# Kernel tuning notes

Measured on AMD Instinct MI355X. Metric: run time of the kernel, lower is better.

Reference implementation:

```python
import jax, jax.numpy as jnp
import numpy as np

N_NODES = 100000
N_EDGES = 1600000
IN_CH, HID_CH, OUT_CH = 128, 64, 40


def setup_inputs() -> dict:
    key = jax.random.key(0)
    k_x, k_e, k_w1, k_w2 = jax.random.split(key, 4)
    x = jax.random.normal(k_x, (N_NODES, IN_CH), dtype=jnp.float32)
    edge_index = jax.random.randint(k_e, (2, N_EDGES), 0, N_NODES, dtype=jnp.int64)
    # Glorot-ish scaled weights, zero bias (matches GCNConv init convention)
    W1 = jax.random.normal(k_w1, (IN_CH, HID_CH), dtype=jnp.float32) / np.sqrt(IN_CH)
    b1 = jnp.zeros((HID_CH,), dtype=jnp.float32)
    W2 = jax.random.normal(k_w2, (HID_CH, OUT_CH), dtype=jnp.float32) / np.sqrt(HID_CH)
    b2 = jnp.zeros((OUT_CH,), dtype=jnp.float32)
    return {"x": x, "edge_index": edge_index, "W1": W1, "b1": b1, "W2": W2, "b2": b2}


def _gcn_conv(x, edge_index, W, b, n):
    """GCNConv with normalize=True: linear transform, add self-loops,
    symmetric D^-1/2 A D^-1/2 aggregation (source_to_target flow), bias."""
    h = x @ W  # [n, out]
    loops = jnp.arange(n, dtype=edge_index.dtype)
    row = jnp.concatenate([edge_index[0], loops])  # sources
    col = jnp.concatenate([edge_index[1], loops])  # targets
    deg = jax.ops.segment_sum(jnp.ones_like(col, dtype=h.dtype), col, num_segments=n)
    dinv = jnp.where(deg > 0, jax.lax.rsqrt(deg), jnp.zeros_like(deg))
    w = dinv[row] * dinv[col]  # [E+n] per-edge norm
    out = jax.ops.segment_sum(h[row] * w[:, None], col, num_segments=n)  # scatter-add to targets
    return out + b


def reference(x, edge_index, W1, b1, W2, b2):
    # eval mode: F.dropout(p=0.8, training=False) is identity
    n = x.shape[0]
    h = jax.nn.relu(_gcn_conv(x, edge_index, W1, b1, n))
    return _gcn_conv(h, edge_index, W2, b2, n)  # [N, OUT_CH] logits
```

## Files before the change

### kernel.cpp

```cpp
#include <hip/hip_runtime.h>

#define N_NODES 100000
#define NPAD    100032
#define N_EDGES 1600000
#define IN_CH   128
#define HID_CH  64
#define OUT_CH  40
#define NBKT    196
#define EPB     4096
#define CAP     9216
#define CAPC    10752

using bf16x8 = __attribute__((ext_vector_type(8))) short;
using f32x4  = __attribute__((ext_vector_type(4))) float;

__device__ __forceinline__ float bf2f(unsigned short u) {
    union { unsigned int i; float f; } c; c.i = ((unsigned int)u) << 16; return c.f;
}
__device__ __forceinline__ unsigned short f2bf(float f) {
    union { float f; unsigned int i; } c; c.f = f;
    unsigned int r = c.i + 0x7FFFu + ((c.i >> 16) & 1u);
    return (unsigned short)(r >> 16);
}
__device__ __forceinline__ float4 bf2f4(ushort4 u) {
    return make_float4(bf2f(u.x), bf2f(u.y), bf2f(u.z), bf2f(u.w));
}

__global__ void k_bin(const int* __restrict__ ei, int* __restrict__ gcur,
                      int* __restrict__ ebuf) {
    __shared__ int hist[NBKT];
    __shared__ int lcur[NBKT];
    int tid = threadIdx.x;
    int base = blockIdx.x * EPB;
    int nloc = N_EDGES - base;
    if (nloc > EPB) nloc = EPB;
    int n4 = nloc >> 2;
    const int4* S4 = (const int4*)(ei + base);
    const int4* D4 = (const int4*)(ei + N_EDGES + base);

    if (tid < NBKT) { hist[tid] = 0; }
    __syncthreads();
    for (int i = tid; i < n4; i += 256) {
        int4 d = D4[i];
        atomicAdd(&hist[d.x >> 9], 1);
        atomicAdd(&hist[d.y >> 9], 1);
        atomicAdd(&hist[d.z >> 9], 1);
        atomicAdd(&hist[d.w >> 9], 1);
    }
    __syncthreads();
    if (tid < NBKT) {
        int h = hist[tid];
        lcur[tid] = h ? (tid * CAP + atomicAdd(&gcur[tid], h)) : 0;
    }
    __syncthreads();
    for (int i = tid; i < n4; i += 256) {
        int4 s = S4[i];
        int4 d = D4[i];
        int p;
        p = atomicAdd(&lcur[d.x >> 9], 1); ebuf[p] = s.x | ((d.x & 511) << 17);
        p = atomicAdd(&lcur[d.y >> 9], 1); ebuf[p] = s.y | ((d.y & 511) << 17);
        p = atomicAdd(&lcur[d.z >> 9], 1); ebuf[p] = s.z | ((d.z & 511) << 17);
        p = atomicAdd(&lcur[d.w >> 9], 1); ebuf[p] = s.w | ((d.w & 511) << 17);
    }
}

__global__ void k_node(const int* __restrict__ gcur, const int* __restrict__ ebuf,
                       int* __restrict__ row_start, int* __restrict__ row_end,
                       int* __restrict__ csr_src, float* __restrict__ dinv) {
    __shared__ int cnt[512];
    __shared__ int s[512];
    int tid = threadIdx.x;
    int b = blockIdx.x;
    int node0 = b << 9;
    int lo = b * CAP;
    int lo2 = b * CAPC;
    int hi = lo + gcur[b];
    int n = hi - lo, n4 = n >> 2;
    const int4* E4 = (const int4*)(ebuf + lo);

    cnt[tid] = 0;
    __syncthreads();
    for (int i = tid; i < n4; i += 512) {
        int4 w = E4[i];
        atomicAdd(&cnt[(unsigned)w.x >> 17], 1);
        atomicAdd(&cnt[(unsigned)w.y >> 17], 1);
        atomicAdd(&cnt[(unsigned)w.z >> 17], 1);
        atomicAdd(&cnt[(unsigned)w.w >> 17], 1);
    }
    for (int e = lo + (n4 << 2) + tid; e < hi; e += 512)
        atomicAdd(&cnt[(unsigned)ebuf[e] >> 17], 1);
    __syncthreads();
    int c = cnt[tid];
    int cp = (c + 7) & ~7;
    s[tid] = cp;
    __syncthreads();
#pragma unroll
    for (int off = 1; off < 512; off <<= 1) {
        int tv = (tid >= off) ? s[tid - off] : 0;
        __syncthreads();
        s[tid] += tv;
        __syncthreads();
    }
    int nodestart = lo2 + s[tid] - cp;
    int node = node0 + tid;
    if (node < N_NODES) {
        row_start[node] = nodestart;
        row_end[node]   = nodestart + c;
        dinv[node] = rsqrtf(1.0f + (float)c);
    }
    __syncthreads();
    cnt[tid] = nodestart;
    __syncthreads();
    for (int i = tid; i < n4; i += 512) {
        int4 w = E4[i];
        int p;
        p = atomicAdd(&cnt[(unsigned)w.x >> 17], 1); csr_src[p] = w.x & 0x1FFFF;
        p = atomicAdd(&cnt[(unsigned)w.y >> 17], 1); csr_src[p] = w.y & 0x1FFFF;
        p = atomicAdd(&cnt[(unsigned)w.z >> 17], 1); csr_src[p] = w.z & 0x1FFFF;
        p = atomicAdd(&cnt[(unsigned)w.w >> 17], 1); csr_src[p] = w.w & 0x1FFFF;
    }
    for (int e = lo + (n4 << 2) + tid; e < hi; e += 512) {
        int w = ebuf[e];
        int p = atomicAdd(&cnt[(unsigned)w >> 17], 1);
        csr_src[p] = w & 0x1FFFF;
    }
    for (int p = nodestart + c; p < nodestart + cp; ++p)
        csr_src[p] = N_NODES;
}

__global__ __launch_bounds__(256, 4)
void k_gemm1(const float* __restrict__ x, const float* __restrict__ W1,
             const float* __restrict__ dinv, unsigned short* __restrict__ h1s) {
    __shared__ unsigned short Bl[64 * 136];
    __shared__ float dl[64];
    int tid = threadIdx.x;
    long long node0 = (long long)blockIdx.x * 64;

    for (int i = tid; i < 128 * 64; i += 256) {
        int k = i >> 6, nn = i & 63;
        Bl[nn * 136 + k] = f2bf(W1[i]);
    }
    if (tid < 64) {
        long long gr = node0 + tid;
        dl[tid] = dinv[gr < N_NODES ? gr : N_NODES - 1];
    }
    __syncthreads();

    int lane = tid & 63, wave = tid >> 6;
    int quad = lane >> 4, l16 = lane & 15;
    int arow = wave * 16 + l16;
    long long ga = node0 + arow;
    if (ga >= N_NODES) ga = N_NODES - 1;
    const float* xr = x + ga * IN_CH;
    f32x4 ac0 = {0,0,0,0}, ac1 = {0,0,0,0}, ac2 = {0,0,0,0}, ac3 = {0,0,0,0};

#pragma unroll
    for (int ks = 0; ks < 4; ++ks) {
        int ko = ks * 32 + quad * 8;
        float4 xa = *(const float4*)&xr[ko];
        float4 xb = *(const float4*)&xr[ko + 4];
        bf16x8 a;
        a[0] = (short)f2bf(xa.x); a[1] = (short)f2bf(xa.y);
        a[2] = (short)f2bf(xa.z); a[3] = (short)f2bf(xa.w);
        a[4] = (short)f2bf(xb.x); a[5] = (short)f2bf(xb.y);
        a[6] = (short)f2bf(xb.z); a[7] = (short)f2bf(xb.w);
        bf16x8 b0 = *(const bf16x8*)&Bl[( 0 + l16) * 136 + ko];
        bf16x8 b1 = *(const bf16x8*)&Bl[(16 + l16) * 136 + ko];
        bf16x8 b2 = *(const bf16x8*)&Bl[(32 + l16) * 136 + ko];
        bf16x8 b3 = *(const bf16x8*)&Bl[(48 + l16) * 136 + ko];
        ac0 = __builtin_amdgcn_mfma_f32_16x16x32_bf16(a, b0, ac0, 0, 0, 0);
        ac1 = __builtin_amdgcn_mfma_f32_16x16x32_bf16(a, b1, ac1, 0, 0, 0);
        ac2 = __builtin_amdgcn_mfma_f32_16x16x32_bf16(a, b2, ac2, 0, 0, 0);
        ac3 = __builtin_amdgcn_mfma_f32_16x16x32_bf16(a, b3, ac3, 0, 0, 0);
    }

#pragma unroll
    for (int r = 0; r < 4; ++r) {
        int rl = wave * 16 + quad * 4 + r;
        long long grow = node0 + rl;
        if (grow < N_NODES) {
            float dd = dl[rl];
            h1s[grow * 64 +  0 + l16] = f2bf(ac0[r] * dd);
            h1s[grow * 64 + 16 + l16] = f2bf(ac1[r] * dd);
            h1s[grow * 64 + 32 + l16] = f2bf(ac2[r] * dd);
            h1s[grow * 64 + 48 + l16] = f2bf(ac3[r] * dd);
        } else {
            h1s[grow * 64 +  0 + l16] = 0;
            h1s[grow * 64 + 16 + l16] = 0;
            h1s[grow * 64 + 32 + l16] = 0;
            h1s[grow * 64 + 48 + l16] = 0;
        }
    }
}

__global__ __launch_bounds__(256, 4)
void k_agg1g2(const int* __restrict__ row_start, const int* __restrict__ row_end,
              const int* __restrict__ csr_src,
              const unsigned short* __restrict__ h1s, const float* __restrict__ dinv,
              const float* __restrict__ b1, const float* __restrict__ W2,
              unsigned short* __restrict__ h2s) {
    __shared__ unsigned short Al[32 * 72];
    __shared__ unsigned short Bl[48 * 72];
    __shared__ float dl[32];
    int tid = threadIdx.x;
    long long node0 = (long long)blockIdx.x * 32;

    for (int i = tid; i < 48 * 64; i += 256) {
        int nn = i >> 6, k = i & 63;
        Bl[nn * 72 + k] = f2bf(nn < OUT_CH ? W2[k * OUT_CH + nn] : 0.0f);
    }
    if (tid < 32) {
        long long gr = node0 + tid;
        dl[tid] = dinv[gr < N_NODES ? gr : N_NODES - 1];
    }
    __syncthreads();

    int g  = tid >> 4;
    int hh = (tid >> 3) & 1;
    int c8 = tid & 7;
    int nl = g * 2 + hh;
    long long node = node0 + nl;

    int e0 = 0, d = 0;
    if (node < N_NODES) { e0 = row_start[node]; d = row_end[node] - e0; }
    int len8 = (d + 7) & ~7;
    int lenO = __shfl_xor(len8, 8, 16);
    int nIt  = (len8 > lenO ? len8 : lenO) >> 3;

    float4 aA = {0.f,0.f,0.f,0.f}, aB = aA, aC = aA, aD = aA;

    int it = 0;
    while (it < nIt) {
        bool real = (it << 3) < len8;
        int base = real ? (e0 + (it << 3)) : e0;
        int idxr = csr_src[base + c8];
        int s0 = __shfl(idxr, 0, 8), s1 = __shfl(idxr, 1, 8);
        int s2 = __shfl(idxr, 2, 8), s3 = __shfl(idxr, 3, 8);
        int s4 = __shfl(idxr, 4, 8), s5 = __shfl(idxr, 5, 8);
        int s6 = __shfl(idxr, 6, 8), s7 = __shfl(idxr, 7, 8);
        if (!real) { s0=s1=s2=s3=s4=s5=s6=s7 = N_NODES; }
        const unsigned short* Hc = h1s + (long long)c8 * 8;
        bf16x8 r0 = *(const bf16x8*)&Hc[(long long)s0 * 64];
        bf16x8 r1 = *(const bf16x8*)&Hc[(long long)s1 * 64];
        bf16x8 r2 = *(const bf16x8*)&Hc[(long long)s2 * 64];
        bf16x8 r3 = *(const bf16x8*)&Hc[(long long)s3 * 64];
        bf16x8 r4 = *(const bf16x8*)&Hc[(long long)s4 * 64];
        bf16x8 r5 = *(const bf16x8*)&Hc[(long long)s5 * 64];
        bf16x8 r6 = *(const bf16x8*)&Hc[(long long)s6 * 64];
        bf16x8 r7 = *(const bf16x8*)&Hc[(long long)s7 * 64];
#define ACC8(R, LO, HI) { \
        LO.x += bf2f((unsigned short)R[0]); LO.y += bf2f((unsigned short)R[1]); \
        LO.z += bf2f((unsigned short)R[2]); LO.w += bf2f((unsigned short)R[3]); \
        HI.x += bf2f((unsigned short)R[4]); HI.y += bf2f((unsigned short)R[5]); \
        HI.z += bf2f((unsigned short)R[6]); HI.w += bf2f((unsigned short)R[7]); }
        ACC8(r0, aA, aB) ACC8(r1, aC, aD)
        ACC8(r2, aA, aB) ACC8(r3, aC, aD)
        ACC8(r4, aA, aB) ACC8(r5, aC, aD)
        ACC8(r6, aA, aB) ACC8(r7, aC, aD)
#undef ACC8
        ++it;
    }
    aA.x += aC.x; aA.y += aC.y; aA.z += aC.z; aA.w += aC.w;
    aB.x += aD.x; aB.y += aD.y; aB.z += aD.z; aB.w += aD.w;

    bf16x8 res = {0,0,0,0,0,0,0,0};
    if (node < N_NODES) {
        bf16x8 sv = *(const bf16x8*)&h1s[(long long)node * 64 + c8 * 8];
        aA.x += bf2f((unsigned short)sv[0]); aA.y += bf2f((unsigned short)sv[1]);
        aA.z += bf2f((unsigned short)sv[2]); aA.w += bf2f((unsigned short)sv[3]);
        aB.x += bf2f((unsigned short)sv[4]); aB.y += bf2f((unsigned short)sv[5]);
        aB.z += bf2f((unsigned short)sv[6]); aB.w += bf2f((unsigned short)sv[7]);
        float dd = dl[nl];
        float4 blo = ((const float4*)b1)[c8 * 2];
        float4 bhi = ((const float4*)b1)[c8 * 2 + 1];
        res[0] = (short)f2bf(fmaxf(aA.x * dd + blo.x, 0.f));
        res[1] = (short)f2bf(fmaxf(aA.y * dd + blo.y, 0.f));
        res[2] = (short)f2bf(fmaxf(aA.z * dd + blo.z, 0.f));
        res[3] = (short)f2bf(fmaxf(aA.w * dd + blo.w, 0.f));
        res[4] = (short)f2bf(fmaxf(aB.x * dd + bhi.x, 0.f));
        res[5] = (short)f2bf(fmaxf(aB.y * dd + bhi.y, 0.f));
        res[6] = (short)f2bf(fmaxf(aB.z * dd + bhi.z, 0.f));
        res[7] = (short)f2bf(fmaxf(aB.w * dd + bhi.w, 0.f));
    }
    *(bf16x8*)&Al[nl * 72 + c8 * 8] = res;
    __syncthreads();

    int lane = tid & 63, wave = tid >> 6;
    if (wave < 2) {
        int quad = lane >> 4, l16 = lane & 15;
        int arow = wave * 16 + l16;
        f32x4 ac0 = {0,0,0,0}, ac1 = {0,0,0,0}, ac2 = {0,0,0,0};

#pragma unroll
        for (int ks = 0; ks < 2; ++ks) {
            int ko = ks * 32 + quad * 8;
            bf16x8 a  = *(const bf16x8*)&Al[arow * 72 + ko];
            bf16x8 b0 = *(const bf16x8*)&Bl[( 0 + l16) * 72 + ko];
            bf16x8 b1v = *(const bf16x8*)&Bl[(16 + l16) * 72 + ko];
            bf16x8 b2 = *(const bf16x8*)&Bl[(32 + l16) * 72 + ko];
            ac0 = __builtin_amdgcn_mfma_f32_16x16x32_bf16(a, b0, ac0, 0, 0, 0);
            ac1 = __builtin_amdgcn_mfma_f32_16x16x32_bf16(a, b1v, ac1, 0, 0, 0);
            ac2 = __builtin_amdgcn_mfma_f32_16x16x32_bf16(a, b2, ac2, 0, 0, 0);
        }

#pragma unroll
        for (int r = 0; r < 4; ++r) {
            int rl = wave * 16 + quad * 4 + r;
            long long grow = node0 + rl;
            if (grow < N_NODES) {
                float dd = dl[rl];
                h2s[grow * 40 +  0 + l16] = f2bf(ac0[r] * dd);
                h2s[grow * 40 + 16 + l16] = f2bf(ac1[r] * dd);
                if (l16 < 8) h2s[grow * 40 + 32 + l16] = f2bf(ac2[r] * dd);
            } else if (grow < NPAD) {
                h2s[grow * 40 +  0 + l16] = 0;
                h2s[grow * 40 + 16 + l16] = 0;
                if (l16 < 8) h2s[grow * 40 + 32 + l16] = 0;
            }
        }
    }
}

__global__ void k_agg2(const int* __restrict__ row_start, const int* __restrict__ row_end,
                       const int* __restrict__ csr_src,
                       const unsigned short* __restrict__ h2s, const float* __restrict__ dinv,
                       const float* __restrict__ b2, float* __restrict__ out) {
    int idx = blockIdx.x * blockDim.x + threadIdx.x;
    int node = idx >> 4;
    int cg = idx & 15;
    if (node >= N_NODES || cg >= 10) return;
    int e = row_start[node];
    int f = row_end[node];
    int f8 = e + ((f - e + 7) & ~7);
    const ushort4* H = (const ushort4*)h2s;
    float4 acc = bf2f4(H[(long long)node * 10 + cg]);
    float4 acc2 = {0.f, 0.f, 0.f, 0.f};
    while (e < f8) {
        int s0 = csr_src[e];
        int s1 = csr_src[e + 1];
        int s2 = csr_src[e + 2];
        int s3 = csr_src[e + 3];
        int s4 = csr_src[e + 4];
        int s5 = csr_src[e + 5];
        int s6 = csr_src[e + 6];
        int s7 = csr_src[e + 7];
        float4 v0 = bf2f4(H[(long long)s0 * 10 + cg]);
        float4 v1 = bf2f4(H[(long long)s1 * 10 + cg]);
        float4 v2 = bf2f4(H[(long long)s2 * 10 + cg]);
        float4 v3 = bf2f4(H[(long long)s3 * 10 + cg]);
        float4 u0 = bf2f4(H[(long long)s4 * 10 + cg]);
        float4 u1 = bf2f4(H[(long long)s5 * 10 + cg]);
        float4 u2 = bf2f4(H[(long long)s6 * 10 + cg]);
        float4 u3 = bf2f4(H[(long long)s7 * 10 + cg]);
        acc.x  += (v0.x + v1.x) + (v2.x + v3.x);
        acc.y  += (v0.y + v1.y) + (v2.y + v3.y);
        acc.z  += (v0.z + v1.z) + (v2.z + v3.z);
        acc.w  += (v0.w + v1.w) + (v2.w + v3.w);
        acc2.x += (u0.x + u1.x) + (u2.x + u3.x);
        acc2.y += (u0.y + u1.y) + (u2.y + u3.y);
        acc2.z += (u0.z + u1.z) + (u2.z + u3.z);
        acc2.w += (u0.w + u1.w) + (u2.w + u3.w);
        e += 8;
    }
    acc.x += acc2.x; acc.y += acc2.y; acc.z += acc2.z; acc.w += acc2.w;
    float dd = dinv[node];
    float4 b = ((const float4*)b2)[cg];
    acc.x = acc.x * dd + b.x;
    acc.y = acc.y * dd + b.y;
    acc.z = acc.z * dd + b.z;
    acc.w = acc.w * dd + b.w;
    ((float4*)out)[(long long)node * 10 + cg] = acc;
}

extern "C" void kernel_launch(void* const* d_in, const int* in_sizes, int n_in,
                              void* d_out, int out_size, void* d_ws, size_t ws_size,
                              hipStream_t stream) {
    const float* x  = (const float*)d_in[0];
    const int*   ei = (const int*)d_in[1];
    const float* W1 = (const float*)d_in[2];
    const float* b1 = (const float*)d_in[3];
    const float* W2 = (const float*)d_in[4];
    const float* b2 = (const float*)d_in[5];
    float* out = (float*)d_out;

    unsigned short* hbuf  = (unsigned short*)d_ws;
    unsigned short* h2buf = hbuf + 64LL * NPAD;
    int* ebuf      = (int*)(h2buf + 40LL * NPAD);
    int* csr_src   = ebuf + NBKT * CAP;
    int* row_start = csr_src + NBKT * CAPC + 64;
    int* row_end   = row_start + N_NODES;
    int* gcur      = row_end + N_NODES;
    float* dinv    = (float*)(gcur + 256);

    const int B = 256;
    const int g16 = (N_NODES * 16 + B - 1) / B;
    const int gRows = NPAD / 64;
    const int gAgg  = NPAD / 32;

    hipMemsetAsync((void*)gcur, 0, NBKT * sizeof(int), stream);
    k_bin<<<(N_EDGES + EPB - 1) / EPB, B, 0, stream>>>(ei, gcur, ebuf);
    k_node<<<NBKT, 512, 0, stream>>>(gcur, ebuf, row_start, row_end, csr_src, dinv);

    k_gemm1<<<gRows, B, 0, stream>>>(x, W1, dinv, hbuf);
    k_agg1g2<<<gAgg, B, 0, stream>>>(row_start, row_end, csr_src, hbuf, dinv,
                                     b1, W2, h2buf);
    k_agg2<<<g16, B, 0, stream>>>(row_start, row_end, csr_src, h2buf, dinv, b2, out);
}
```

Measured before the change: 215.8 us.

## Restructure layer-2 aggregation with 16-byte gathers and shuffled edge indices

Rewrites k_agg2 so each node uses 8 lanes, 5 of them active, and each lane loads 8 bf16 values (16 bytes) instead of 4. The lanes load 8 neighbour indices cooperatively in one coalesced read and broadcast them with width-8 shuffles, so each lane no longer fetches every index itself. Two nodes share a 16-lane group and loop to the longer of their two edge counts, so the shorter node issues padded dummy gathers. Those dummy loads, and the ones from the 3 idle lanes, point at the zeroed padding row N_NODES, so they add nothing to the sums. Block count drops to NPAD/32 blocks of 32 nodes, with launch bounds added.

Result: no change. 215.1 us (-0.3%).

```diff
diff --git a/kernel.cpp b/kernel.cpp
--- a/kernel.cpp
+++ b/kernel.cpp
@@ -321,55 +321,84 @@
     }
 }
 
-__global__ void k_agg2(const int* __restrict__ row_start, const int* __restrict__ row_end,
-                       const int* __restrict__ csr_src,
-                       const unsigned short* __restrict__ h2s, const float* __restrict__ dinv,
-                       const float* __restrict__ b2, float* __restrict__ out) {
-    int idx = blockIdx.x * blockDim.x + threadIdx.x;
-    int node = idx >> 4;
-    int cg = idx & 15;
-    if (node >= N_NODES || cg >= 10) return;
-    int e = row_start[node];
-    int f = row_end[node];
-    int f8 = e + ((f - e + 7) & ~7);
-    const ushort4* H = (const ushort4*)h2s;
-    float4 acc = bf2f4(H[(long long)node * 10 + cg]);
-    float4 acc2 = {0.f, 0.f, 0.f, 0.f};
-    while (e < f8) {
-        int s0 = csr_src[e];
-        int s1 = csr_src[e + 1];
-        int s2 = csr_src[e + 2];
-        int s3 = csr_src[e + 3];
-        int s4 = csr_src[e + 4];
-        int s5 = csr_src[e + 5];
-        int s6 = csr_src[e + 6];
-        int s7 = csr_src[e + 7];
-        float4 v0 = bf2f4(H[(long long)s0 * 10 + cg]);
-        float4 v1 = bf2f4(H[(long long)s1 * 10 + cg]);
-        float4 v2 = bf2f4(H[(long long)s2 * 10 + cg]);
-        float4 v3 = bf2f4(H[(long long)s3 * 10 + cg]);
-        float4 u0 = bf2f4(H[(long long)s4 * 10 + cg]);
-        float4 u1 = bf2f4(H[(long long)s5 * 10 + cg]);
-        float4 u2 = bf2f4(H[(long long)s6 * 10 + cg]);
-        float4 u3 = bf2f4(H[(long long)s7 * 10 + cg]);
-        acc.x  += (v0.x + v1.x) + (v2.x + v3.x);
-        acc.y  += (v0.y + v1.y) + (v2.y + v3.y);
-        acc.z  += (v0.z + v1.z) + (v2.z + v3.z);
-        acc.w  += (v0.w + v1.w) + (v2.w + v3.w);
-        acc2.x += (u0.x + u1.x) + (u2.x + u3.x);
-        acc2.y += (u0.y + u1.y) + (u2.y + u3.y);
-        acc2.z += (u0.z + u1.z) + (u2.z + u3.z);
-        acc2.w += (u0.w + u1.w) + (u2.w + u3.w);
-        e += 8;
-    }
-    acc.x += acc2.x; acc.y += acc2.y; acc.z += acc2.z; acc.w += acc2.w;
-    float dd = dinv[node];
-    float4 b = ((const float4*)b2)[cg];
-    acc.x = acc.x * dd + b.x;
-    acc.y = acc.y * dd + b.y;
-    acc.z = acc.z * dd + b.z;
-    acc.w = acc.w * dd + b.w;
-    ((float4*)out)[(long long)node * 10 + cg] = acc;
+__global__ __launch_bounds__(256, 4)
+void k_agg2(const int* __restrict__ row_start, const int* __restrict__ row_end,
+            const int* __restrict__ csr_src,
+            const unsigned short* __restrict__ h2s, const float* __restrict__ dinv,
+            const float* __restrict__ b2, float* __restrict__ out) {
+    int tid = threadIdx.x;
+    long long node0 = (long long)blockIdx.x * 32;
+
+    int g  = tid >> 4;
+    int hh = (tid >> 3) & 1;
+    int c8 = tid & 7;
+    int nl = g * 2 + hh;
+    long long node = node0 + nl;
+    bool act = c8 < 5;
+
+    int e0 = 0, d = 0;
+    if (node < N_NODES) { e0 = row_start[node]; d = row_end[node] - e0; }
+    int len8 = (d + 7) & ~7;
+    int lenO = __shfl_xor(len8, 8, 16);
+    int nIt  = (len8 > lenO ? len8 : lenO) >> 3;
+
+    const unsigned short* Hb = h2s + (act ? (long long)c8 * 8
+                                          : (long long)N_NODES * 40);
+    long long rmul = act ? 40LL : 0LL;
+
+    float4 aA = {0.f,0.f,0.f,0.f}, aB = aA, aC = aA, aD = aA;
+
+    int it = 0;
+    while (it < nIt) {
+        bool real = (it << 3) < len8;
+        int base = real ? (e0 + (it << 3)) : e0;
+        int idxr = csr_src[base + c8];
+        int s0 = __shfl(idxr, 0, 8), s1 = __shfl(idxr, 1, 8);
+        int s2 = __shfl(idxr, 2, 8), s3 = __shfl(idxr, 3, 8);
+        int s4 = __shfl(idxr, 4, 8), s5 = __shfl(idxr, 5, 8);
+        int s6 = __shfl(idxr, 6, 8), s7 = __shfl(idxr, 7, 8);
+        if (!real) { s0=s1=s2=s3=s4=s5=s6=s7 = N_NODES; }
+        bf16x8 r0 = *(const bf16x8*)&Hb[(long long)s0 * rmul];
+        bf16x8 r1 = *(const bf16x8*)&Hb[(long long)s1 * rmul];
+        bf16x8 r2 = *(const bf16x8*)&Hb[(long long)s2 * rmul];
+        bf16x8 r3 = *(const bf16x8*)&Hb[(long long)s3 * rmul];
+        bf16x8 r4 = *(const bf16x8*)&Hb[(long long)s4 * rmul];
+        bf16x8 r5 = *(const bf16x8*)&Hb[(long long)s5 * rmul];
+        bf16x8 r6 = *(const bf16x8*)&Hb[(long long)s6 * rmul];
+        bf16x8 r7 = *(const bf16x8*)&Hb[(long long)s7 * rmul];
+#define ACC8(R, LO, HI) { \
+        LO.x += bf2f((unsigned short)R[0]); LO.y += bf2f((unsigned short)R[1]); \
+        LO.z += bf2f((unsigned short)R[2]); LO.w += bf2f((unsigned short)R[3]); \
+        HI.x += bf2f((unsigned short)R[4]); HI.y += bf2f((unsigned short)R[5]); \
+        HI.z += bf2f((unsigned short)R[6]); HI.w += bf2f((unsigned short)R[7]); }
+        ACC8(r0, aA, aB) ACC8(r1, aC, aD)
+        ACC8(r2, aA, aB) ACC8(r3, aC, aD)
+        ACC8(r4, aA, aB) ACC8(r5, aC, aD)
+        ACC8(r6, aA, aB) ACC8(r7, aC, aD)
+#undef ACC8
+        ++it;
+    }
+    aA.x += aC.x; aA.y += aC.y; aA.z += aC.z; aA.w += aC.w;
+    aB.x += aD.x; aB.y += aD.y; aB.z += aD.z; aB.w += aD.w;
+
+    if (node < N_NODES && act) {
+        bf16x8 sv = *(const bf16x8*)&h2s[(long long)node * 40 + c8 * 8];
+        aA.x += bf2f((unsigned short)sv[0]); aA.y += bf2f((unsigned short)sv[1]);
+        aA.z += bf2f((unsigned short)sv[2]); aA.w += bf2f((unsigned short)sv[3]);
+        aB.x += bf2f((unsigned short)sv[4]); aB.y += bf2f((unsigned short)sv[5]);
+        aB.z += bf2f((unsigned short)sv[6]); aB.w += bf2f((unsigned short)sv[7]);
+        float dd = dinv[node];
+        float4 blo = ((const float4*)b2)[c8 * 2];
+        float4 bhi = ((const float4*)b2)[c8 * 2 + 1];
+        float4 o0, o1;
+        o0.x = aA.x * dd + blo.x; o0.y = aA.y * dd + blo.y;
+        o0.z = aA.z * dd + blo.z; o0.w = aA.w * dd + blo.w;
+        o1.x = aB.x * dd + bhi.x; o1.y = aB.y * dd + bhi.y;
+        o1.z = aB.z * dd + bhi.z; o1.w = aB.w * dd + bhi.w;
+        float* op = out + node * 40 + c8 * 8;
+        *(float4*)op = o0;
+        *(float4*)(op + 4) = o1;
+    }
 }
 
 extern "C" void kernel_launch(void* const* d_in, const int* in_sizes, int n_in,
@@ -393,7 +422,6 @@
     float* dinv    = (float*)(gcur + 256);
 
     const int B = 256;
-    const int g16 = (N_NODES * 16 + B - 1) / B;
     const int gRows = NPAD / 64;
     const int gAgg  = NPAD / 32;
 
@@ -404,5 +432,5 @@
     k_gemm1<<<gRows, B, 0, stream>>>(x, W1, dinv, hbuf);
     k_agg1g2<<<gAgg, B, 0, stream>>>(row_start, row_end, csr_src, hbuf, dinv,
                                      b1, W2, h2buf);
-    k_agg2<<<g16, B, 0, stream>>>(row_start, row_end, csr_src, h2buf, dinv, b2, out);
-}
+    k_agg2<<<gAgg, B, 0, stream>>>(row_start, row_end, csr_src, h2buf, dinv, b2, out);
+}
```
